# Performance work log

Hardware: AMD Instinct MI355X
Metric: run time of the kernel (lower is better)

## Reference

```python
import jax, jax.numpy as jnp
import numpy as np

L, D, H, FF, WS2 = 2, 768, 12, 3072, 49  # nlayer, hidden_dim, nhead, ff_dim, win_size**2
DH = D // H
EPS = 1e-5


def _ln(x, w, b):
    m = jnp.mean(x, axis=-1, keepdims=True)
    v = jnp.mean((x - m) ** 2, axis=-1, keepdims=True)
    return (x - m) * jax.lax.rsqrt(v + EPS) * w + b


def setup_inputs() -> dict:
    key = jax.random.key(0)
    ks = jax.random.split(key, 12)
    s = 0.02
    return {
        "x": jax.random.normal(ks[0], (8, 3136, D), dtype=jnp.float32),
        "Wqkv": jax.random.normal(ks[1], (L, 3 * D, D), dtype=jnp.float32) * s,
        "bqkv": jnp.zeros((L, 3 * D), dtype=jnp.float32),
        "Wo": jax.random.normal(ks[2], (L, D, D), dtype=jnp.float32) * s,
        "bo": jnp.zeros((L, D), dtype=jnp.float32),
        "ln1_w": jnp.ones((L, D), dtype=jnp.float32),
        "ln1_b": jnp.zeros((L, D), dtype=jnp.float32),
        "W1": jax.random.normal(ks[3], (L, FF, D), dtype=jnp.float32) * s,
        "b1": jnp.zeros((L, FF), dtype=jnp.float32),
        "W2": jax.random.normal(ks[4], (L, D, FF), dtype=jnp.float32) * s,
        "b2": jnp.zeros((L, D), dtype=jnp.float32),
        "ln2_w": jnp.ones((L, D), dtype=jnp.float32),
        "ln2_b": jnp.zeros((L, D), dtype=jnp.float32),
    }


def reference(x, Wqkv, bqkv, Wo, bo, ln1_w, ln1_b, W1, b1, W2, b2, ln2_w, ln2_b):
    B, S, _ = x.shape
    nwin = S // WS2
    # windowed batching: each contiguous 49-token chunk is an independent sequence
    h = x.reshape(B * nwin, WS2, D)
    scale = 1.0 / jnp.sqrt(jnp.asarray(DH, dtype=h.dtype))
    for l in range(L):
        # pre-norm self-attention
        y = _ln(h, ln1_w[l], ln1_b[l])
        qkv = y @ Wqkv[l].T + bqkv[l]                      # [N, WS2, 3D]
        q, k, v = jnp.split(qkv, 3, axis=-1)
        q = q.reshape(-1, WS2, H, DH)
        k = k.reshape(-1, WS2, H, DH)
        v = v.reshape(-1, WS2, H, DH)
        scores = jnp.einsum('bqhd,bkhd->bhqk', q, k) * scale
        attn = jax.nn.softmax(scores, axis=-1)
        o = jnp.einsum('bhqk,bkhd->bqhd', attn, v).reshape(-1, WS2, D)
        h = h + o @ Wo[l].T + bo[l]
        # pre-norm FFN with exact GELU
        y = _ln(h, ln2_w[l], ln2_b[l])
        h = h + jax.nn.gelu(y @ W1[l].T + b1[l], approximate=False) @ W2[l].T + b2[l]
    return h.reshape(B, S, D)
```

## Files before the change

### kernel.cpp

```cpp
#include <hip/hip_runtime.h>

#define MTOT 25088
#define DMODEL 768
#define NH 12
#define WIN 49
#define NLAYER 2

typedef short bf16x8 __attribute__((ext_vector_type(8)));
typedef float f32x4 __attribute__((ext_vector_type(4)));
typedef unsigned short u16x4 __attribute__((ext_vector_type(4)));

__device__ __forceinline__ float bf2f(short s) {
    return __uint_as_float(((unsigned)(unsigned short)s) << 16);
}
__device__ __forceinline__ short f2b(float f) {
    unsigned x = __float_as_uint(f);
    unsigned r = x + 0x7FFFu + ((x >> 16) & 1u);
    return (short)(r >> 16);
}

__global__ __launch_bounds__(256) void cvt_f32_to_bf16(const float* __restrict__ in,
                                                       short* __restrict__ out, int n8) {
    int i = blockIdx.x * 256 + threadIdx.x;
    if (i >= n8) return;
    const float4* p = (const float4*)in + (size_t)i * 2;
    float4 a = p[0], b = p[1];
    bf16x8 o;
    o[0] = f2b(a.x); o[1] = f2b(a.y); o[2] = f2b(a.z); o[3] = f2b(a.w);
    o[4] = f2b(b.x); o[5] = f2b(b.y); o[6] = f2b(b.z); o[7] = f2b(b.w);
    *((bf16x8*)out + i) = o;
}

__global__ __launch_bounds__(256) void ln_to_bf16(const float* __restrict__ h,
                                                  const float* __restrict__ w,
                                                  const float* __restrict__ b,
                                                  short* __restrict__ y) {
    int wave = threadIdx.x >> 6, lane = threadIdx.x & 63;
    int row = blockIdx.x * 4 + wave;
    const float4* hp = (const float4*)(h + (size_t)row * DMODEL);
    float4 v[3];
    float s = 0.f, s2 = 0.f;
#pragma unroll
    for (int c = 0; c < 3; c++) {
        v[c] = hp[lane + 64 * c];
        s += v[c].x + v[c].y + v[c].z + v[c].w;
        s2 += v[c].x * v[c].x + v[c].y * v[c].y + v[c].z * v[c].z + v[c].w * v[c].w;
    }
#pragma unroll
    for (int off = 32; off > 0; off >>= 1) {
        s += __shfl_xor(s, off);
        s2 += __shfl_xor(s2, off);
    }
    float mean = s * (1.f / DMODEL);
    float var = s2 * (1.f / DMODEL) - mean * mean;
    float rstd = rsqrtf(var + 1e-5f);
#pragma unroll
    for (int c = 0; c < 3; c++) {
        float4 wv = ((const float4*)w)[lane + 64 * c];
        float4 bv = ((const float4*)b)[lane + 64 * c];
        u16x4 o;
        o[0] = (unsigned short)f2b((v[c].x - mean) * rstd * wv.x + bv.x);
        o[1] = (unsigned short)f2b((v[c].y - mean) * rstd * wv.y + bv.y);
        o[2] = (unsigned short)f2b((v[c].z - mean) * rstd * wv.z + bv.z);
        o[3] = (unsigned short)f2b((v[c].w - mean) * rstd * wv.w + bv.w);
        *(u16x4*)(y + (size_t)row * DMODEL + (size_t)(lane + 64 * c) * 4) = o;
    }
}

template <int EPI>
__global__ __launch_bounds__(256, 2)
void gemm_bt(const short* __restrict__ A, const short* __restrict__ B,
             const float* __restrict__ bias, void* __restrict__ C,
             int M, int N, int K) {
    __shared__ __align__(16) short As[128 * 32];
    __shared__ __align__(16) short Bs[128 * 32];
    const int tid = threadIdx.x;
    const int wave = tid >> 6, lane = tid & 63;
    const int row0 = blockIdx.y * 128, col0 = blockIdx.x * 128;
    const int wm = (wave >> 1) * 64, wn = (wave & 1) * 64;
    const int rq = lane >> 4, fr = lane & 15;

    f32x4 acc[4][4] = {};

    const int srow = wave * 32 + (lane >> 2);
    const int scol = (lane & 3) * 8;
    const short* Ag = A + (size_t)row0 * K;
    const short* Bg = B + (size_t)col0 * K;

    for (int kt = 0; kt < K; kt += 32) {
#pragma unroll
        for (int i = 0; i < 2; i++) {
            __builtin_amdgcn_global_load_lds(
                (const __attribute__((address_space(1))) void*)(Ag + (size_t)(srow + i * 16) * K + kt + scol),
                (__attribute__((address_space(3))) void*)(As + (wave * 2 + i) * 512),
                16, 0, 0);
            __builtin_amdgcn_global_load_lds(
                (const __attribute__((address_space(1))) void*)(Bg + (size_t)(srow + i * 16) * K + kt + scol),
                (__attribute__((address_space(3))) void*)(Bs + (wave * 2 + i) * 512),
                16, 0, 0);
        }
        __syncthreads();
        bf16x8 af[4], bfr[4];
#pragma unroll
        for (int i = 0; i < 4; i++)
            af[i] = *(const bf16x8*)(As + (wm + i * 16 + fr) * 32 + rq * 8);
#pragma unroll
        for (int n = 0; n < 4; n++)
            bfr[n] = *(const bf16x8*)(Bs + (wn + n * 16 + fr) * 32 + rq * 8);
#pragma unroll
        for (int i = 0; i < 4; i++)
#pragma unroll
            for (int n = 0; n < 4; n++)
                acc[i][n] = __builtin_amdgcn_mfma_f32_16x16x32_bf16(af[i], bfr[n], acc[i][n], 0, 0, 0);
        __syncthreads();
    }

#pragma unroll
    for (int i = 0; i < 4; i++) {
#pragma unroll
        for (int n = 0; n < 4; n++) {
            int col = col0 + wn + n * 16 + fr;
            float bv = bias[col];
#pragma unroll
            for (int r = 0; r < 4; r++) {
                int row = row0 + wm + i * 16 + rq * 4 + r;
                size_t idx = (size_t)row * N + col;
                float v = acc[i][n][r] + bv;
                if (EPI == 0) {
                    ((short*)C)[idx] = f2b(v);
                } else if (EPI == 1) {
                    float* O = (float*)C;
                    O[idx] = O[idx] + v;
                } else {
                    float g = 0.5f * v * (1.0f + erff(v * 0.70710678118654752f));
                    ((short*)C)[idx] = f2b(g);
                }
            }
        }
    }
}

__global__ __launch_bounds__(64) void attn_win(const short* __restrict__ qkv,
                                               short* __restrict__ out) {
    const int win = blockIdx.x / NH;
    const int head = blockIdx.x % NH;
    __shared__ __align__(16) short Ks[WIN * 64];
    __shared__ __align__(16) short Vs[WIN * 64];
    __shared__ float Ps[64 * WIN];
    const int lane = threadIdx.x;
    const size_t rb = (size_t)win * WIN;
    const int qoff = head * 64;

    for (int i = lane; i < WIN * 8; i += 64) {
        int r = i >> 3, c = (i & 7) * 8;
        const short* kg = qkv + (rb + r) * 2304 + DMODEL + qoff + c;
        *(bf16x8*)(Ks + r * 64 + c) = *(const bf16x8*)kg;
        *(bf16x8*)(Vs + r * 64 + c) = *(const bf16x8*)(kg + DMODEL);
    }
    __syncthreads();
    if (lane < WIN) {
        float q[64];
        const short* qg = qkv + (rb + lane) * 2304 + qoff;
#pragma unroll
        for (int c = 0; c < 8; c++) {
            bf16x8 t = *(const bf16x8*)(qg + c * 8);
#pragma unroll
            for (int d = 0; d < 8; d++) q[c * 8 + d] = bf2f(t[d]);
        }
        float m = -1e30f;
        for (int j = 0; j < WIN; j++) {
            float a = 0.f;
#pragma unroll
            for (int c = 0; c < 8; c++) {
                bf16x8 kv = *(const bf16x8*)(Ks + j * 64 + c * 8);
#pragma unroll
                for (int d = 0; d < 8; d++) a += q[c * 8 + d] * bf2f(kv[d]);
            }
            a *= 0.125f;
            Ps[lane * WIN + j] = a;
            m = fmaxf(m, a);
        }
        float sum = 0.f;
        for (int j = 0; j < WIN; j++) {
            float p = __expf(Ps[lane * WIN + j] - m);
            Ps[lane * WIN + j] = p;
            sum += p;
        }
        float rinv = 1.f / sum;
        short* og = out + (rb + lane) * DMODEL + qoff;
        for (int c = 0; c < 8; c++) {
            float o[8] = {0.f, 0.f, 0.f, 0.f, 0.f, 0.f, 0.f, 0.f};
            for (int j = 0; j < WIN; j++) {
                float p = Ps[lane * WIN + j];
                bf16x8 vv = *(const bf16x8*)(Vs + j * 64 + c * 8);
#pragma unroll
                for (int d = 0; d < 8; d++) o[d] += p * bf2f(vv[d]);
            }
            bf16x8 ov;
#pragma unroll
            for (int d = 0; d < 8; d++) ov[d] = f2b(o[d] * rinv);
            *(bf16x8*)(og + c * 8) = ov;
        }
    }
}

extern "C" void kernel_launch(void* const* d_in, const int* in_sizes, int n_in,
                              void* d_out, int out_size, void* d_ws, size_t ws_size,
                              hipStream_t stream) {
    const float* x    = (const float*)d_in[0];
    const float* Wqkv = (const float*)d_in[1];
    const float* bqkv = (const float*)d_in[2];
    const float* Wo   = (const float*)d_in[3];
    const float* bo   = (const float*)d_in[4];
    const float* ln1w = (const float*)d_in[5];
    const float* ln1b = (const float*)d_in[6];
    const float* W1   = (const float*)d_in[7];
    const float* b1   = (const float*)d_in[8];
    const float* W2   = (const float*)d_in[9];
    const float* b2   = (const float*)d_in[10];
    const float* ln2w = (const float*)d_in[11];
    const float* ln2b = (const float*)d_in[12];

    const int M = MTOT;
    char* ws = (char*)d_ws;
    short* ybf   = (short*)(ws);
    short* bigbf = (short*)(ws + 38535168);
    short* wqkvb = (short*)(ws + 38535168 + 154140672);
    short* wob   = wqkvb + (size_t)NLAYER * 2304 * 768;
    short* w1b   = wob + (size_t)NLAYER * 768 * 768;
    short* w2b   = w1b + (size_t)NLAYER * 3072 * 768;

    hipMemcpyAsync(d_out, (const void*)x, (size_t)M * DMODEL * sizeof(float),
                   hipMemcpyDeviceToDevice, stream);

    {
        size_t n;
        n = (size_t)NLAYER * 2304 * 768;
        cvt_f32_to_bf16<<<((int)(n / 8) + 255) / 256, 256, 0, stream>>>(Wqkv, wqkvb, (int)(n / 8));
        n = (size_t)NLAYER * 768 * 768;
        cvt_f32_to_bf16<<<((int)(n / 8) + 255) / 256, 256, 0, stream>>>(Wo, wob, (int)(n / 8));
        n = (size_t)NLAYER * 3072 * 768;
        cvt_f32_to_bf16<<<((int)(n / 8) + 255) / 256, 256, 0, stream>>>(W1, w1b, (int)(n / 8));
        n = (size_t)NLAYER * 768 * 3072;
        cvt_f32_to_bf16<<<((int)(n / 8) + 255) / 256, 256, 0, stream>>>(W2, w2b, (int)(n / 8));
    }

    float* h = (float*)d_out;
    for (int l = 0; l < NLAYER; l++) {
        ln_to_bf16<<<M / 4, 256, 0, stream>>>(h, ln1w + l * DMODEL, ln1b + l * DMODEL, ybf);
        {
            dim3 g(2304 / 128, M / 128);
            gemm_bt<0><<<g, 256, 0, stream>>>(ybf, wqkvb + (size_t)l * 2304 * 768,
                                              bqkv + (size_t)l * 2304, bigbf, M, 2304, DMODEL);
        }
        attn_win<<<(M / WIN) * NH, 64, 0, stream>>>(bigbf, ybf);
        {
            dim3 g(768 / 128, M / 128);
            gemm_bt<1><<<g, 256, 0, stream>>>(ybf, wob + (size_t)l * 768 * 768,
                                              bo + (size_t)l * 768, h, M, 768, DMODEL);
        }
        ln_to_bf16<<<M / 4, 256, 0, stream>>>(h, ln2w + l * DMODEL, ln2b + l * DMODEL, ybf);
        {
            dim3 g(3072 / 128, M / 128);
            gemm_bt<2><<<g, 256, 0, stream>>>(ybf, w1b + (size_t)l * 3072 * 768,
                                              b1 + (size_t)l * 3072, bigbf, M, 3072, DMODEL);
        }
        {
            dim3 g(768 / 128, M / 128);
            gemm_bt<1><<<g, 256, 0, stream>>>(bigbf, w2b + (size_t)l * 768 * 3072,
                                              b2 + (size_t)l * 768, h, M, 768, 3072);
        }
    }
}
```

Before: 1.859 ms.

## Replace 128x128 GEMM with pipelined 256-wide tile kernel with XCD remap

Replaces the simple single-buffered 128x128 bf16 GEMM with a 512-thread kernel using 256x256 or 128x256 tiles, a K step of 64 split into halves, and double-buffered LDS filled by direct global-to-LDS loads. The loads for the next stages are issued while MFMAs run, with explicit vmcnt/lgkmcnt waits and barriers, and s_setprio raised around the MFMA blocks. It also uses XOR-swizzled LDS addressing to avoid bank conflicts and remaps block IDs across the 8 XCDs for cache locality. The aim is to hide global-load latency and raise MFMA utilisation. In exchange it uses much more LDS per block, depends on fragile hand-tuned wait counts, and has fewer blocks for the N=768 GEMMs.

```diff
diff --git a/kernel.cpp b/kernel.cpp
--- a/kernel.cpp
+++ b/kernel.cpp
@@ -67,68 +67,137 @@
     }
 }
 
-template <int EPI>
-__global__ __launch_bounds__(256, 2)
-void gemm_bt(const short* __restrict__ A, const short* __restrict__ B,
+#define BAR() asm volatile("s_barrier" ::: "memory")
+#define LGKM0() do { asm volatile("s_waitcnt lgkmcnt(0)" ::: "memory"); __builtin_amdgcn_sched_barrier(0); } while (0)
+
+template <int EPI, int MF>
+__global__ __launch_bounds__(512, 2)
+void gemm256(const short* __restrict__ A, const short* __restrict__ B,
              const float* __restrict__ bias, void* __restrict__ C,
-             int M, int N, int K) {
-    __shared__ __align__(16) short As[128 * 32];
-    __shared__ __align__(16) short Bs[128 * 32];
+             int N, int K, int gx) {
+    constexpr int ABYTES = MF * 2048;
+    constexpr int BSOFF = 4 * ABYTES;
+    __shared__ char lds[BSOFF + 65536];
     const int tid = threadIdx.x;
     const int wave = tid >> 6, lane = tid & 63;
-    const int row0 = blockIdx.y * 128, col0 = blockIdx.x * 128;
-    const int wm = (wave >> 1) * 64, wn = (wave & 1) * 64;
-    const int rq = lane >> 4, fr = lane & 15;
-
-    f32x4 acc[4][4] = {};
-
-    const int srow = wave * 32 + (lane >> 2);
-    const int scol = (lane & 3) * 8;
+    const int wr = wave >> 2, wc = wave & 3;
+    const int fr = lane & 15, rq = lane >> 4;
+
+    int nwg = gridDim.x, orig = blockIdx.x;
+    int q8 = nwg >> 3, r8 = nwg & 7;
+    int xcd = orig & 7, lid = orig >> 3;
+    int wg = (xcd < r8 ? xcd * (q8 + 1) : r8 * (q8 + 1) + (xcd - r8) * q8) + lid;
+    const int bn = wg % gx, bm = wg / gx;
+    const int row0 = bm * (MF * 32), col0 = bn * 256;
+    const int nt = K >> 6;
+
     const short* Ag = A + (size_t)row0 * K;
     const short* Bg = B + (size_t)col0 * K;
 
-    for (int kt = 0; kt < K; kt += 32) {
-#pragma unroll
-        for (int i = 0; i < 2; i++) {
-            __builtin_amdgcn_global_load_lds(
-                (const __attribute__((address_space(1))) void*)(Ag + (size_t)(srow + i * 16) * K + kt + scol),
-                (__attribute__((address_space(3))) void*)(As + (wave * 2 + i) * 512),
-                16, 0, 0);
-            __builtin_amdgcn_global_load_lds(
-                (const __attribute__((address_space(1))) void*)(Bg + (size_t)(srow + i * 16) * K + kt + scol),
-                (__attribute__((address_space(3))) void*)(Bs + (wave * 2 + i) * 512),
-                16, 0, 0);
-        }
-        __syncthreads();
-        bf16x8 af[4], bfr[4];
-#pragma unroll
-        for (int i = 0; i < 4; i++)
-            af[i] = *(const bf16x8*)(As + (wm + i * 16 + fr) * 32 + rq * 8);
-#pragma unroll
-        for (int n = 0; n < 4; n++)
-            bfr[n] = *(const bf16x8*)(Bs + (wn + n * 16 + fr) * 32 + rq * 8);
-#pragma unroll
-        for (int i = 0; i < 4; i++)
-#pragma unroll
-            for (int n = 0; n < 4; n++)
-                acc[i][n] = __builtin_amdgcn_mfma_f32_16x16x32_bf16(af[i], bfr[n], acc[i][n], 0, 0, 0);
-        __syncthreads();
-    }
-
-#pragma unroll
-    for (int i = 0; i < 4; i++) {
+#define STAGE_A(T, KH) do { int ts_ = ((T) < nt ? (T) : 0);                                        \
+    _Pragma("unroll") for (int j = 0; j < MF / 4; j++) {                                           \
+      int rr_ = (tid >> 2) + j * 128;                                                              \
+      int ch_ = (tid & 3) ^ ((rr_ >> 1) & 3);                                                      \
+      __builtin_amdgcn_global_load_lds(                                                            \
+        (const __attribute__((address_space(1))) void*)(Ag + (size_t)rr_ * K + ts_ * 64 + (KH) * 32 + ch_ * 8), \
+        (__attribute__((address_space(3))) void*)(lds + ((((T) & 1) * 2 * ABYTES) + (KH) * ABYTES + wave * 1024 + j * 8192)), \
+        16, 0, 0); } } while (0)
+
+#define STAGE_B(T, KH) do { int ts_ = ((T) < nt ? (T) : 0);                                        \
+    _Pragma("unroll") for (int j = 0; j < 2; j++) {                                                \
+      int rr_ = (tid >> 2) + j * 128;                                                              \
+      int ch_ = (tid & 3) ^ ((rr_ >> 1) & 3);                                                      \
+      __builtin_amdgcn_global_load_lds(                                                            \
+        (const __attribute__((address_space(1))) void*)(Bg + (size_t)rr_ * K + ts_ * 64 + (KH) * 32 + ch_ * 8), \
+        (__attribute__((address_space(3))) void*)(lds + (BSOFF + (((T) & 1) * 32768) + (KH) * 16384 + wave * 1024 + j * 8192)), \
+        16, 0, 0); } } while (0)
+
+#define LDA(m, KH, BUF) (*(const bf16x8*)(lds + (((BUF) * 2 * ABYTES) + (KH) * ABYTES +            \
+    (((wr * (MF * 16) + (m) * 16 + fr) * 64 + rq * 16) ^ ((((wr * (MF * 16) + (m) * 16 + fr) >> 1) & 3) << 4)))))
+#define LDB(n, KH, BUF) (*(const bf16x8*)(lds + (BSOFF + ((BUF) * 32768) + (KH) * 16384 +          \
+    (((wc * 64 + (n) * 16 + fr) * 64 + rq * 16) ^ ((((wc * 64 + (n) * 16 + fr) >> 1) & 3) << 4)))))
+
+#define VMW() do { if constexpr (MF == 8) asm volatile("s_waitcnt vmcnt(8)" ::: "memory");         \
+                   else                   asm volatile("s_waitcnt vmcnt(6)" ::: "memory"); } while (0)
+
+    f32x4 acc[MF][4] = {};
+
+    STAGE_A(0, 0); STAGE_B(0, 0);
+    STAGE_A(0, 1); STAGE_B(0, 1);
+    STAGE_A(1, 0); STAGE_B(1, 0);
+    VMW();
+    BAR();
+
+    for (int t = 0; t < nt; t++) {
+        const int buf = t & 1;
+        bf16x8 a[MF], b0, b1, b2, b3;
+#pragma unroll
+        for (int m = 0; m < MF; m++) a[m] = LDA(m, 0, buf);
+        b0 = LDB(0, 0, buf); b1 = LDB(1, 0, buf);
+        STAGE_A(t + 1, 1);
+        BAR(); LGKM0();
+        __builtin_amdgcn_s_setprio(1);
+#pragma unroll
+        for (int m = 0; m < MF; m++) {
+            acc[m][0] = __builtin_amdgcn_mfma_f32_16x16x32_bf16(a[m], b0, acc[m][0], 0, 0, 0);
+            acc[m][1] = __builtin_amdgcn_mfma_f32_16x16x32_bf16(a[m], b1, acc[m][1], 0, 0, 0);
+        }
+        __builtin_amdgcn_s_setprio(0);
+        BAR();
+        b2 = LDB(2, 0, buf); b3 = LDB(3, 0, buf);
+        STAGE_B(t + 1, 1);
+        VMW();
+        BAR(); LGKM0();
+        __builtin_amdgcn_s_setprio(1);
+#pragma unroll
+        for (int m = 0; m < MF; m++) {
+            acc[m][2] = __builtin_amdgcn_mfma_f32_16x16x32_bf16(a[m], b2, acc[m][2], 0, 0, 0);
+            acc[m][3] = __builtin_amdgcn_mfma_f32_16x16x32_bf16(a[m], b3, acc[m][3], 0, 0, 0);
+        }
+        __builtin_amdgcn_s_setprio(0);
+        BAR();
+#pragma unroll
+        for (int m = 0; m < MF; m++) a[m] = LDA(m, 1, buf);
+        b0 = LDB(0, 1, buf); b1 = LDB(1, 1, buf);
+        STAGE_A(t + 2, 0);
+        BAR(); LGKM0();
+        __builtin_amdgcn_s_setprio(1);
+#pragma unroll
+        for (int m = 0; m < MF; m++) {
+            acc[m][0] = __builtin_amdgcn_mfma_f32_16x16x32_bf16(a[m], b0, acc[m][0], 0, 0, 0);
+            acc[m][1] = __builtin_amdgcn_mfma_f32_16x16x32_bf16(a[m], b1, acc[m][1], 0, 0, 0);
+        }
+        __builtin_amdgcn_s_setprio(0);
+        BAR();
+        b2 = LDB(2, 1, buf); b3 = LDB(3, 1, buf);
+        STAGE_B(t + 2, 0);
+        VMW();
+        BAR(); LGKM0();
+        __builtin_amdgcn_s_setprio(1);
+#pragma unroll
+        for (int m = 0; m < MF; m++) {
+            acc[m][2] = __builtin_amdgcn_mfma_f32_16x16x32_bf16(a[m], b2, acc[m][2], 0, 0, 0);
+            acc[m][3] = __builtin_amdgcn_mfma_f32_16x16x32_bf16(a[m], b3, acc[m][3], 0, 0, 0);
+        }
+        __builtin_amdgcn_s_setprio(0);
+        BAR();
+    }
+    asm volatile("s_waitcnt vmcnt(0)" ::: "memory");
+
+#pragma unroll
+    for (int m = 0; m < MF; m++) {
 #pragma unroll
         for (int n = 0; n < 4; n++) {
-            int col = col0 + wn + n * 16 + fr;
+            int col = col0 + wc * 64 + n * 16 + fr;
             float bv = bias[col];
 #pragma unroll
-            for (int r = 0; r < 4; r++) {
-                int row = row0 + wm + i * 16 + rq * 4 + r;
+            for (int rg = 0; rg < 4; rg++) {
+                int row = row0 + wr * (MF * 16) + m * 16 + rq * 4 + rg;
                 size_t idx = (size_t)row * N + col;
-                float v = acc[i][n][r] + bv;
-                if (EPI == 0) {
+                float v = acc[m][n][rg] + bv;
+                if constexpr (EPI == 0) {
                     ((short*)C)[idx] = f2b(v);
-                } else if (EPI == 1) {
+                } else if constexpr (EPI == 1) {
                     float* O = (float*)C;
                     O[idx] = O[idx] + v;
                 } else {
@@ -138,6 +207,11 @@
             }
         }
     }
+#undef STAGE_A
+#undef STAGE_B
+#undef LDA
+#undef LDB
+#undef VMW
 }
 
 __global__ __launch_bounds__(64) void attn_win(const short* __restrict__ qkv,
@@ -248,27 +322,15 @@
     float* h = (float*)d_out;
     for (int l = 0; l < NLAYER; l++) {
         ln_to_bf16<<<M / 4, 256, 0, stream>>>(h, ln1w + l * DMODEL, ln1b + l * DMODEL, ybf);
-        {
-            dim3 g(2304 / 128, M / 128);
-            gemm_bt<0><<<g, 256, 0, stream>>>(ybf, wqkvb + (size_t)l * 2304 * 768,
-                                              bqkv + (size_t)l * 2304, bigbf, M, 2304, DMODEL);
-        }
+        gemm256<0, 8><<<dim3(9 * 98), 512, 0, stream>>>(
+            ybf, wqkvb + (size_t)l * 2304 * 768, bqkv + (size_t)l * 2304, bigbf, 2304, 768, 9);
         attn_win<<<(M / WIN) * NH, 64, 0, stream>>>(bigbf, ybf);
-        {
-            dim3 g(768 / 128, M / 128);
-            gemm_bt<1><<<g, 256, 0, stream>>>(ybf, wob + (size_t)l * 768 * 768,
-                                              bo + (size_t)l * 768, h, M, 768, DMODEL);
-        }
+        gemm256<1, 4><<<dim3(3 * 196), 512, 0, stream>>>(
+            ybf, wob + (size_t)l * 768 * 768, bo + (size_t)l * 768, h, 768, 768, 3);
         ln_to_bf16<<<M / 4, 256, 0, stream>>>(h, ln2w + l * DMODEL, ln2b + l * DMODEL, ybf);
-        {
-            dim3 g(3072 / 128, M / 128);
-            gemm_bt<2><<<g, 256, 0, stream>>>(ybf, w1b + (size_t)l * 3072 * 768,
-                                              b1 + (size_t)l * 3072, bigbf, M, 3072, DMODEL);
-        }
-        {
-            dim3 g(768 / 128, M / 128);
-            gemm_bt<1><<<g, 256, 0, stream>>>(bigbf, w2b + (size_t)l * 768 * 3072,
-                                              b2 + (size_t)l * 768, h, M, 768, 3072);
-        }
-    }
-}
+        gemm256<2, 8><<<dim3(12 * 98), 512, 0, stream>>>(
+            ybf, w1b + (size_t)l * 3072 * 768, b1 + (size_t)l * 3072, bigbf, 3072, 768, 12);
+        gemm256<1, 4><<<dim3(3 * 196), 512, 0, stream>>>(
+            bigbf, w2b + (size_t)l * 768 * 3072, b2 + (size_t)l * 768, h, 768, 3072, 3);
+    }
+}
```

New measurement: 1.822 ms. 2.0% less time.

## Rewrite GEMM with 256x128 tiles, double-buffered LDS, swizzle and XCD remap

Applied to the files above, without the earlier changes.

Replaces the single-buffered 128x128 GEMM with a 256x128 tile kernel. It double-buffers global-to-LDS loads so the next K-slice is fetched while MFMAs run, XOR-swizzles LDS columns to avoid bank conflicts, and remaps block IDs so neighbouring tiles share an XCD for better L2 reuse. It also raises wave priority around the MFMA block. The larger accumulator (32 f32x4 per thread) and 48KB of LDS raise register and LDS pressure, which may limit occupancy. The edge tile is handled by clamping the stage index.

```diff
diff --git a/kernel.cpp b/kernel.cpp
--- a/kernel.cpp
+++ b/kernel.cpp
@@ -67,68 +67,96 @@
     }
 }
 
+#define BAR() asm volatile("s_barrier" ::: "memory")
+#define LGKM0() do { asm volatile("s_waitcnt lgkmcnt(0)" ::: "memory"); __builtin_amdgcn_sched_barrier(0); } while (0)
+
 template <int EPI>
 __global__ __launch_bounds__(256, 2)
-void gemm_bt(const short* __restrict__ A, const short* __restrict__ B,
-             const float* __restrict__ bias, void* __restrict__ C,
-             int M, int N, int K) {
-    __shared__ __align__(16) short As[128 * 32];
-    __shared__ __align__(16) short Bs[128 * 32];
+void gemm_u(const short* __restrict__ A, const short* __restrict__ B,
+            const float* __restrict__ bias, void* __restrict__ C,
+            int N, int K, int gx) {
+    __shared__ char lds[49152];
     const int tid = threadIdx.x;
     const int wave = tid >> 6, lane = tid & 63;
-    const int row0 = blockIdx.y * 128, col0 = blockIdx.x * 128;
-    const int wm = (wave >> 1) * 64, wn = (wave & 1) * 64;
-    const int rq = lane >> 4, fr = lane & 15;
-
-    f32x4 acc[4][4] = {};
-
-    const int srow = wave * 32 + (lane >> 2);
-    const int scol = (lane & 3) * 8;
+    const int wr = wave >> 1, wc = wave & 1;
+    const int fr = lane & 15, rq = lane >> 4;
+
+    int nwg = gridDim.x, orig = blockIdx.x;
+    int q8 = nwg >> 3, r8 = nwg & 7;
+    int xcd = orig & 7, lid = orig >> 3;
+    int wg = (xcd < r8 ? xcd * (q8 + 1) : r8 * (q8 + 1) + (xcd - r8) * q8) + lid;
+    const int bn = wg % gx, bm = wg / gx;
+    const int row0 = bm * 256, col0 = bn * 128;
+    const int nt = K >> 5;
+
     const short* Ag = A + (size_t)row0 * K;
     const short* Bg = B + (size_t)col0 * K;
-
-    for (int kt = 0; kt < K; kt += 32) {
-#pragma unroll
-        for (int i = 0; i < 2; i++) {
-            __builtin_amdgcn_global_load_lds(
-                (const __attribute__((address_space(1))) void*)(Ag + (size_t)(srow + i * 16) * K + kt + scol),
-                (__attribute__((address_space(3))) void*)(As + (wave * 2 + i) * 512),
-                16, 0, 0);
-            __builtin_amdgcn_global_load_lds(
-                (const __attribute__((address_space(1))) void*)(Bg + (size_t)(srow + i * 16) * K + kt + scol),
-                (__attribute__((address_space(3))) void*)(Bs + (wave * 2 + i) * 512),
-                16, 0, 0);
-        }
-        __syncthreads();
-        bf16x8 af[4], bfr[4];
-#pragma unroll
-        for (int i = 0; i < 4; i++)
-            af[i] = *(const bf16x8*)(As + (wm + i * 16 + fr) * 32 + rq * 8);
-#pragma unroll
-        for (int n = 0; n < 4; n++)
-            bfr[n] = *(const bf16x8*)(Bs + (wn + n * 16 + fr) * 32 + rq * 8);
-#pragma unroll
-        for (int i = 0; i < 4; i++)
+    const int lrow = lane >> 2;
+    const int lcol = ((lane & 3) ^ (lrow & 3)) * 8;
+
+#define STAGE(T) do { int ts_ = ((T) < nt ? (T) : (nt - 1));                                       \
+    _Pragma("unroll") for (int j = 0; j < 4; j++) {                                                \
+      int seg_ = wave * 4 + j;                                                                     \
+      __builtin_amdgcn_global_load_lds(                                                            \
+        (const __attribute__((address_space(1))) void*)(Ag + (size_t)(seg_ * 16 + lrow) * K + ts_ * 32 + lcol), \
+        (__attribute__((address_space(3))) void*)(lds + (((T) & 1) * 16384 + seg_ * 1024)),        \
+        16, 0, 0); }                                                                               \
+    _Pragma("unroll") for (int j = 0; j < 2; j++) {                                                \
+      int seg_ = wave * 2 + j;                                                                     \
+      __builtin_amdgcn_global_load_lds(                                                            \
+        (const __attribute__((address_space(1))) void*)(Bg + (size_t)(seg_ * 16 + lrow) * K + ts_ * 32 + lcol), \
+        (__attribute__((address_space(3))) void*)(lds + (32768 + ((T) & 1) * 8192 + seg_ * 1024)), \
+        16, 0, 0); } } while (0)
+
+#define LDA(m, BUF) (*(const bf16x8*)(lds + ((BUF) * 16384 +                                        \
+    (wr * 128 + (m) * 16 + fr) * 64 + ((rq * 16) ^ ((fr & 3) << 4)))))
+#define LDB(n, BUF) (*(const bf16x8*)(lds + (32768 + (BUF) * 8192 +                                 \
+    (wc * 64 + (n) * 16 + fr) * 64 + ((rq * 16) ^ ((fr & 3) << 4)))))
+
+    f32x4 acc[8][4] = {};
+
+    STAGE(0);
+    STAGE(1);
+    asm volatile("s_waitcnt vmcnt(6)" ::: "memory");
+    BAR();
+
+    for (int t = 0; t < nt; t++) {
+        const int buf = t & 1;
+        bf16x8 a[8], b[4];
+#pragma unroll
+        for (int m = 0; m < 8; m++) a[m] = LDA(m, buf);
+#pragma unroll
+        for (int n = 0; n < 4; n++) b[n] = LDB(n, buf);
+        LGKM0();
+        BAR();
+        STAGE(t + 2);
+        __builtin_amdgcn_s_setprio(1);
+#pragma unroll
+        for (int m = 0; m < 8; m++) {
 #pragma unroll
             for (int n = 0; n < 4; n++)
-                acc[i][n] = __builtin_amdgcn_mfma_f32_16x16x32_bf16(af[i], bfr[n], acc[i][n], 0, 0, 0);
-        __syncthreads();
-    }
-
-#pragma unroll
-    for (int i = 0; i < 4; i++) {
+                acc[m][n] = __builtin_amdgcn_mfma_f32_16x16x32_bf16(a[m], b[n], acc[m][n], 0, 0, 0);
+        }
+        __builtin_amdgcn_s_setprio(0);
+        asm volatile("s_waitcnt vmcnt(6)" ::: "memory");
+        BAR();
+    }
+    asm volatile("s_waitcnt vmcnt(0)" ::: "memory");
+
+#pragma unroll
+    for (int m = 0; m < 8; m++) {
 #pragma unroll
         for (int n = 0; n < 4; n++) {
-            int col = col0 + wn + n * 16 + fr;
+            int col = col0 + wc * 64 + n * 16 + fr;
             float bv = bias[col];
 #pragma unroll
-            for (int r = 0; r < 4; r++) {
-                int row = row0 + wm + i * 16 + rq * 4 + r;
+            for (int rg = 0; rg < 4; rg++) {
+                int row = row0 + wr * 128 + m * 16 + rq * 4 + rg;
                 size_t idx = (size_t)row * N + col;
-                float v = acc[i][n][r] + bv;
-                if (EPI == 0) {
+                float v = acc[m][n][rg] + bv;
+                if constexpr (EPI == 0) {
                     ((short*)C)[idx] = f2b(v);
-                } else if (EPI == 1) {
+                } else if constexpr (EPI == 1) {
                     float* O = (float*)C;
                     O[idx] = O[idx] + v;
                 } else {
@@ -138,6 +166,9 @@
             }
         }
     }
+#undef STAGE
+#undef LDA
+#undef LDB
 }
 
 __global__ __launch_bounds__(64) void attn_win(const short* __restrict__ qkv,
@@ -248,27 +279,15 @@
     float* h = (float*)d_out;
     for (int l = 0; l < NLAYER; l++) {
         ln_to_bf16<<<M / 4, 256, 0, stream>>>(h, ln1w + l * DMODEL, ln1b + l * DMODEL, ybf);
-        {
-            dim3 g(2304 / 128, M / 128);
-            gemm_bt<0><<<g, 256, 0, stream>>>(ybf, wqkvb + (size_t)l * 2304 * 768,
-                                              bqkv + (size_t)l * 2304, bigbf, M, 2304, DMODEL);
-        }
+        gemm_u<0><<<dim3(18 * 98), 256, 0, stream>>>(
+            ybf, wqkvb + (size_t)l * 2304 * 768, bqkv + (size_t)l * 2304, bigbf, 2304, 768, 18);
         attn_win<<<(M / WIN) * NH, 64, 0, stream>>>(bigbf, ybf);
-        {
-            dim3 g(768 / 128, M / 128);
-            gemm_bt<1><<<g, 256, 0, stream>>>(ybf, wob + (size_t)l * 768 * 768,
-                                              bo + (size_t)l * 768, h, M, 768, DMODEL);
-        }
+        gemm_u<1><<<dim3(6 * 98), 256, 0, stream>>>(
+            ybf, wob + (size_t)l * 768 * 768, bo + (size_t)l * 768, h, 768, 768, 6);
         ln_to_bf16<<<M / 4, 256, 0, stream>>>(h, ln2w + l * DMODEL, ln2b + l * DMODEL, ybf);
-        {
-            dim3 g(3072 / 128, M / 128);
-            gemm_bt<2><<<g, 256, 0, stream>>>(ybf, w1b + (size_t)l * 3072 * 768,
-                                              b1 + (size_t)l * 3072, bigbf, M, 3072, DMODEL);
-        }
-        {
-            dim3 g(768 / 128, M / 128);
-            gemm_bt<1><<<g, 256, 0, stream>>>(bigbf, w2b + (size_t)l * 768 * 3072,
-                                              b2 + (size_t)l * 768, h, M, 768, 3072);
-        }
-    }
-}
+        gemm_u<2><<<dim3(24 * 98), 256, 0, stream>>>(
+            ybf, w1b + (size_t)l * 3072 * 768, b1 + (size_t)l * 3072, bigbf, 3072, 768, 24);
+        gemm_u<1><<<dim3(6 * 98), 256, 0, stream>>>(
+            bigbf, w2b + (size_t)l * 768 * 3072, b2 + (size_t)l * 768, h, 768, 3072, 6);
+    }
+}
```

New measurement: 1.894 ms. No clear change (+1.9%).
